# Kernel optimization log

Measured on AMD Instinct MI355X. Metric: run time of the kernel, lower is better.

Reference implementation:

```python
import jax, jax.numpy as jnp
import numpy as np

N_E = 1024
E_DIM = 256
N_TOK = 262144


def setup_inputs() -> dict:
    key = jax.random.key(0)
    kx, kw = jax.random.split(key)
    x = jax.random.normal(kx, (N_TOK, E_DIM), dtype=jnp.float32)
    # nn.Embedding weight init: uniform(-1/n_e, 1/n_e)
    emb = jax.random.uniform(kw, (N_E, E_DIM), dtype=jnp.float32,
                             minval=-1.0 / N_E, maxval=1.0 / N_E)
    return {"x": x, "emb": emb}


def reference(x, emb):
    # d[n, k] = ||x_n||^2 + ||e_k||^2 - 2 <x_n, e_k>   -> [N, n_e]
    d = (jnp.sum(x * x, axis=1, keepdims=True)
         + jnp.sum(emb * emb, axis=1)
         - 2.0 * jnp.matmul(x, emb.T))
    min_indices = jnp.argmin(d, axis=1)          # [N] int
    z_q = jnp.take(emb, min_indices, axis=0)     # [N, e_dim]
    return z_q, min_indices
```

## Files before the change

### kernel.cpp

```cpp
#include <hip/hip_runtime.h>


constexpr int N_E   = 1024;
constexpr int E_DIM = 256;
constexpr int N_TOK = 262144;
constexpr float THR = 3e-4f;
constexpr int RGRID  = 1024;
constexpr int RRANGE = N_TOK / RGRID;

typedef __attribute__((ext_vector_type(8))) short short8;
typedef __attribute__((ext_vector_type(4))) float f32x4;

__device__ __forceinline__ float sqf(float v) {
    float p = v * v;
    asm volatile("" : "+v"(p));
    return p;
}
__device__ __forceinline__ float pwb(const float* b, int n) {
    float U[8];
#pragma unroll
    for (int L = 0; L < 8; ++L) {
        float TL  = (sqf(b[L])     + sqf(b[16 + L])) + (sqf(b[32 + L]) + sqf(b[48 + L]));
        float TL8 = (sqf(b[8 + L]) + sqf(b[24 + L])) + (sqf(b[40 + L]) + sqf(b[56 + L]));
        U[L] = TL + TL8;
    }
    float V0 = U[0] + U[4], V1 = U[1] + U[5], V2 = U[2] + U[6], V3 = U[3] + U[7];
    float res = (V0 + V2) + (V1 + V3);
    for (int i = 64; i < n; ++i) res += sqf(b[i]);
    return res;
}
__device__ __forceinline__ float rowsq_exact(const float* r) {
    return sqf(r[0]) + (pwb(r + 1, 120) + (pwb(r + 121, 64) + pwb(r + 185, 71)));
}
__device__ __forceinline__ unsigned short f2bf(float f) {
    union { float f; unsigned u; } v; v.f = f;
    unsigned r = (v.u + 0x7FFF + ((v.u >> 16) & 1)) >> 16;
    return (unsigned short)r;
}

__global__ __launch_bounds__(64) void rowsq_kernel(const float* __restrict__ src,
                                                   float* __restrict__ dst) {
    __shared__ float rs[32][257];
    const int rowBase = blockIdx.x * 32;
    const int tid = threadIdx.x;
    const float4* s4 = reinterpret_cast<const float4*>(src);
    for (int i = tid; i < 32 * 64; i += 64) {
        int rr = i >> 6, c4 = i & 63;
        float4 v = s4[(size_t)(rowBase + rr) * 64 + c4];
        rs[rr][c4 * 4 + 0] = v.x;
        rs[rr][c4 * 4 + 1] = v.y;
        rs[rr][c4 * 4 + 2] = v.z;
        rs[rr][c4 * 4 + 3] = v.w;
    }
    __syncthreads();
    if (tid < 32) dst[rowBase + tid] = rowsq_exact(rs[tid]);
}

__global__ __launch_bounds__(256) void eprep_kernel(const float* __restrict__ emb,
                                                    short8* __restrict__ eb,
                                                    int* __restrict__ cnt) {
    int gid = blockIdx.x * 256 + threadIdx.x;
    if (gid == 0) *cnt = 0;
    int lane = gid & 63;
    int kc   = (gid >> 6) & 7;
    int nt   = gid >> 9;
    int cand = nt * 16 + (lane & 15);
    int k0   = kc * 32 + (lane >> 4) * 8;
    const float4* e4 = reinterpret_cast<const float4*>(emb);
    float4 a = e4[(size_t)cand * 64 + k0 / 4];
    float4 b = e4[(size_t)cand * 64 + k0 / 4 + 1];
    short8 o;
    o[0] = (short)f2bf(a.x); o[1] = (short)f2bf(a.y);
    o[2] = (short)f2bf(a.z); o[3] = (short)f2bf(a.w);
    o[4] = (short)f2bf(b.x); o[5] = (short)f2bf(b.y);
    o[6] = (short)f2bf(b.z); o[7] = (short)f2bf(b.w);
    eb[gid] = o;
}

__device__ __forceinline__ void top2_update(const f32x4& acc0, const f32x4& acc1,
                                            float Bv, int idx,
                                            float* m1, float* m2, int* i1) {
#pragma unroll
    for (int mt = 0; mt < 2; ++mt) {
        const f32x4& acc = mt ? acc1 : acc0;
#pragma unroll
        for (int r = 0; r < 4; ++r) {
            int t = mt * 4 + r;
            float s = Bv - 2.0f * acc[r];
            bool lt = s < m1[t];
            m2[t] = lt ? m1[t] : fminf(m2[t], s);
            m1[t] = lt ? s : m1[t];
            i1[t] = lt ? idx : i1[t];
        }
    }
}

__global__ __launch_bounds__(256, 4) void score_kernel(const float* __restrict__ x,
                                                       const float* __restrict__ emb,
                                                       const short8* __restrict__ eb,
                                                       const float* __restrict__ B,
                                                       float* __restrict__ zq,
                                                       float* __restrict__ outIdx,
                                                       int* __restrict__ cnt,
                                                       int* __restrict__ list,
                                                       int listCap) {
    __shared__ short8 esm[2][512];
    __shared__ int fidx[128];
    const int tid = threadIdx.x;
    const int wv  = tid >> 6;
    const int l   = tid & 63;
    const int col = l & 15;
    const int tokW = blockIdx.x * 128 + wv * 32;
    const float4* x4 = reinterpret_cast<const float4*>(x);

    short8 xf[2][8];
#pragma unroll
    for (int mt = 0; mt < 2; ++mt) {
        int row = tokW + mt * 16 + col;
#pragma unroll
        for (int kc = 0; kc < 8; ++kc) {
            const float4* p = x4 + (size_t)row * 64 + kc * 8 + (l >> 4) * 2;
            float4 a = p[0], b = p[1];
            short8 f;
            f[0] = (short)f2bf(a.x); f[1] = (short)f2bf(a.y);
            f[2] = (short)f2bf(a.z); f[3] = (short)f2bf(a.w);
            f[4] = (short)f2bf(b.x); f[5] = (short)f2bf(b.y);
            f[6] = (short)f2bf(b.z); f[7] = (short)f2bf(b.w);
            xf[mt][kc] = f;
        }
    }

    float m1[8], m2[8];
    int   i1[8];
#pragma unroll
    for (int t = 0; t < 8; ++t) { m1[t] = 3.4e38f; m2[t] = 3.4e38f; i1[t] = 0; }

    {
        short8 r0 = eb[tid];
        short8 r1 = eb[256 + tid];
        esm[0][tid]       = r0;
        esm[0][256 + tid] = r1;
    }
    __syncthreads();

    int cur = 0;
    for (int nt = 0; nt < 64; ++nt) {
        short8 p0, p1;
        if (nt < 63) {
            p0 = eb[(nt + 1) * 512 + tid];
            p1 = eb[(nt + 1) * 512 + 256 + tid];
        }
        float Bv = B[nt * 16 + col];
        f32x4 acc0 = {0.f, 0.f, 0.f, 0.f}, acc1 = acc0;
#pragma unroll
        for (int kc = 0; kc < 8; ++kc) {
            short8 ef = esm[cur][kc * 64 + l];
            acc0 = __builtin_amdgcn_mfma_f32_16x16x32_bf16(xf[0][kc], ef, acc0, 0, 0, 0);
            acc1 = __builtin_amdgcn_mfma_f32_16x16x32_bf16(xf[1][kc], ef, acc1, 0, 0, 0);
        }
        top2_update(acc0, acc1, Bv, nt * 16 + col, m1, m2, i1);
        if (nt < 63) {
            esm[cur ^ 1][tid]       = p0;
            esm[cur ^ 1][256 + tid] = p1;
            __syncthreads();
            cur ^= 1;
        }
    }

#pragma unroll
    for (int off = 1; off <= 8; off <<= 1) {
#pragma unroll
        for (int t = 0; t < 8; ++t) {
            float om1 = __shfl_xor(m1[t], off, 64);
            int   oi  = __shfl_xor(i1[t], off, 64);
            float om2 = __shfl_xor(m2[t], off, 64);
            float nm2 = fminf(fmaxf(m1[t], om1), fminf(m2[t], om2));
            if (om1 < m1[t] || (om1 == m1[t] && oi < i1[t])) { m1[t] = om1; i1[t] = oi; }
            m2[t] = nm2;
        }
    }

    if (col == 0) {
        int g = l >> 4;
#pragma unroll
        for (int mt = 0; mt < 2; ++mt)
#pragma unroll
            for (int r = 0; r < 4; ++r) {
                int t = mt * 4 + r;
                int token = tokW + mt * 16 + g * 4 + r;
                int fl = (m2[t] - m1[t] <= THR) ? 1 : 0;
                outIdx[token] = (float)(i1[t] + (fl ? N_E : 0));
                fidx[wv * 32 + mt * 16 + g * 4 + r] = i1[t];
                if (fl) {
                    int p = atomicAdd(cnt, 1);
                    if (p < listCap) list[p] = token;
                }
            }
    }
    __syncthreads();

    const float4* e4 = reinterpret_cast<const float4*>(emb);
    float4* zq4 = reinterpret_cast<float4*>(zq);
#pragma unroll
    for (int it = 0; it < 32; ++it) {
        int flat = it * 256 + tid;
        int t = flat >> 6, c = flat & 63;
        zq4[((size_t)blockIdx.x * 128 + t) * 64 + c] = e4[(size_t)fidx[t] * 64 + c];
    }
}

__device__ __forceinline__ void process_batch(const float4* x4, const float4* e4,
                                              const float* B, float4* zq4,
                                              float* outIdx,
                                              const int* toks, int m,
                                              float (*xs)[260], float* As,
                                              float (*wmin)[16], int (*widx)[16],
                                              int* bidx, int tid, int wv, int l) {
    for (int i = tid; i < 16 * 64; i += 256) {
        int t = i >> 6, c4 = i & 63;
        float4 v = {0.f, 0.f, 0.f, 0.f};
        if (t < m) v = x4[(size_t)toks[t] * 64 + c4];
        *reinterpret_cast<float4*>(&xs[t][c4 * 4]) = v;
    }
    __syncthreads();
    if (tid < 16) As[tid] = rowsq_exact(xs[tid]);
    __syncthreads();

    const float4* er[4];
#pragma unroll
    for (int j = 0; j < 4; ++j) er[j] = e4 + (size_t)(j * 256 + tid) * 64;

    float acc[16][4];
#pragma unroll
    for (int t = 0; t < 16; ++t)
#pragma unroll
        for (int j = 0; j < 4; ++j) acc[t][j] = 0.f;

    for (int ch = 0; ch < 32; ++ch) {
        float ee[4][8];
#pragma unroll
        for (int j = 0; j < 4; ++j) {
            float4 a = er[j][ch * 2 + 0];
            float4 b = er[j][ch * 2 + 1];
            ee[j][0] = a.x; ee[j][1] = a.y; ee[j][2] = a.z; ee[j][3] = a.w;
            ee[j][4] = b.x; ee[j][5] = b.y; ee[j][6] = b.z; ee[j][7] = b.w;
        }
#pragma unroll
        for (int t = 0; t < 16; ++t) {
            float4 xa = *reinterpret_cast<const float4*>(&xs[t][ch * 8 + 0]);
            float4 xb = *reinterpret_cast<const float4*>(&xs[t][ch * 8 + 4]);
            float xv[8] = {xa.x, xa.y, xa.z, xa.w, xb.x, xb.y, xb.z, xb.w};
#pragma unroll
            for (int j = 0; j < 4; ++j) {
                acc[t][j] += xv[0] * ee[j][0];
                acc[t][j] += xv[1] * ee[j][1];
                acc[t][j] += xv[2] * ee[j][2];
                acc[t][j] += xv[3] * ee[j][3];
                acc[t][j] += xv[4] * ee[j][4];
                acc[t][j] += xv[5] * ee[j][5];
                acc[t][j] += xv[6] * ee[j][6];
                acc[t][j] += xv[7] * ee[j][7];
            }
        }
    }

    float m1[16];
    int   i1[16];
#pragma unroll
    for (int t = 0; t < 16; ++t) { m1[t] = 3.4e38f; i1[t] = 0; }
#pragma unroll
    for (int j = 0; j < 4; ++j) {
        int c = j * 256 + tid;
        float Bc = B[c];
#pragma unroll
        for (int t = 0; t < 16; ++t) {
            float tt = As[t] + Bc;
            float s  = tt - 2.0f * acc[t][j];
            if (s < m1[t]) { m1[t] = s; i1[t] = c; }
        }
    }
#pragma unroll
    for (int off = 1; off <= 32; off <<= 1) {
#pragma unroll
        for (int t = 0; t < 16; ++t) {
            float om = __shfl_xor(m1[t], off, 64);
            int   oi = __shfl_xor(i1[t], off, 64);
            if (om < m1[t] || (om == m1[t] && oi < i1[t])) { m1[t] = om; i1[t] = oi; }
        }
    }
    if (l == 0) {
#pragma unroll
        for (int t = 0; t < 16; ++t) { wmin[wv][t] = m1[t]; widx[wv][t] = i1[t]; }
    }
    __syncthreads();
    if (tid < 16) {
        float bm = wmin[0][tid];
        int   bi = widx[0][tid];
#pragma unroll
        for (int w = 1; w < 4; ++w) {
            float om = wmin[w][tid];
            int   oi = widx[w][tid];
            if (om < bm || (om == bm && oi < bi)) { bm = om; bi = oi; }
        }
        bidx[tid] = bi;
        if (tid < m) outIdx[toks[tid]] = (float)bi;
    }
    __syncthreads();
    for (int i = tid; i < m * 64; i += 256) {
        int t = i >> 6, c4 = i & 63;
        zq4[(size_t)toks[t] * 64 + c4] = e4[(size_t)bidx[t] * 64 + c4];
    }
    __syncthreads();
}

__global__ __launch_bounds__(256) void recheck_kernel(const float* __restrict__ x,
                                                      const float* __restrict__ emb,
                                                      const float* __restrict__ B,
                                                      float* __restrict__ zq,
                                                      float* __restrict__ outIdx,
                                                      const int* __restrict__ cnt,
                                                      const int* __restrict__ list,
                                                      int listCap) {
    __shared__ float xs[16][260];
    __shared__ float As[16];
    __shared__ float wmin[4][16];
    __shared__ int   widx[4][16];
    __shared__ int   bidx[16];
    __shared__ int   lt[RRANGE];
    __shared__ int   kcount;

    const int tid = threadIdx.x;
    const int wv  = tid >> 6;
    const int l   = tid & 63;
    const float4* x4 = reinterpret_cast<const float4*>(x);
    const float4* e4 = reinterpret_cast<const float4*>(emb);
    float4* zq4 = reinterpret_cast<float4*>(zq);

    const int n = *cnt;
    if (n == 0) return;

    if (n <= listCap) {
        const int nsb = (n + 15) >> 4;
        for (int sb = blockIdx.x; sb < nsb; sb += gridDim.x) {
            const int m = (n - sb * 16 < 16) ? (n - sb * 16) : 16;
            if (tid < m) lt[tid] = list[sb * 16 + tid];
            __syncthreads();
            process_batch(x4, e4, B, zq4, outIdx, lt, m,
                          xs, As, wmin, widx, bidx, tid, wv, l);
        }
    } else {
        const int base = blockIdx.x * RRANGE;
        if (tid == 0) kcount = 0;
        __syncthreads();
        for (int i = tid; i < RRANGE; i += 256) {
            float v = outIdx[base + i];
            if (v >= (float)N_E) {
                int p = atomicAdd(&kcount, 1);
                lt[p] = base + i;
            }
        }
        __syncthreads();
        const int k = kcount;
        for (int sb = 0; sb < k; sb += 16) {
            const int m = (k - sb < 16) ? (k - sb) : 16;
            process_batch(x4, e4, B, zq4, outIdx, lt + sb, m,
                          xs, As, wmin, widx, bidx, tid, wv, l);
        }
    }
}

extern "C" void kernel_launch(void* const* d_in, const int* in_sizes, int n_in,
                              void* d_out, int out_size, void* d_ws, size_t ws_size,
                              hipStream_t stream) {
    const float* x   = (const float*)d_in[0];
    const float* emb = (const float*)d_in[1];
    float* out    = (float*)d_out;
    float* zq     = out;
    float* outIdx = out + (size_t)N_TOK * E_DIM;

    char* ws = (char*)d_ws;
    int*    cnt  = (int*)ws;
    float*  B    = (float*)(ws + 4096);
    short8* eb   = (short8*)(ws + 8192);
    int*    list = (int*)(ws + 8192 + 524288);
    long avail = (long)ws_size - (8192 + 524288);
    int listCap = avail > 0 ? (int)(avail / 4) : 0;
    if (listCap > N_TOK) listCap = N_TOK;

    eprep_kernel<<<128, 256, 0, stream>>>(emb, eb, cnt);
    rowsq_kernel<<<N_E / 32, 64, 0, stream>>>(emb, B);
    score_kernel<<<N_TOK / 128, 256, 0, stream>>>(x, emb, eb, B, zq, outIdx, cnt, list, listCap);
    recheck_kernel<<<RGRID, 256, 0, stream>>>(x, emb, B, zq, outIdx, cnt, list, listCap);
}
```

Measured before the change: 476.8 us.

## Cull recheck candidates with bf16 MFMA prefilter before exact fp32 rescoring

In the recheck pass, ambiguous tokens are first scored against all codes with bf16 MFMA. Only codes within a margin of the approximate minimum are kept as candidates, and those few are rescored exactly in fp32. This replaces a full fp32 distance computation over all 1024 codes for each flagged token. If any token has more than 64 candidates, the batch falls back to the full path, and the margin has to cover bf16 error for the result to stay exact.

```diff
diff --git a/kernel.cpp b/kernel.cpp
--- a/kernel.cpp
+++ b/kernel.cpp
@@ -4,9 +4,11 @@
 constexpr int N_E   = 1024;
 constexpr int E_DIM = 256;
 constexpr int N_TOK = 262144;
-constexpr float THR = 3e-4f;
+constexpr float THR  = 3e-4f;
+constexpr float CULL = 6e-4f;
 constexpr int RGRID  = 1024;
 constexpr int RRANGE = N_TOK / RGRID;
+constexpr int CMAX   = 64;
 
 typedef __attribute__((ext_vector_type(8))) short short8;
 typedef __attribute__((ext_vector_type(4))) float f32x4;
@@ -209,13 +211,13 @@
     }
 }
 
-__device__ __forceinline__ void process_batch(const float4* x4, const float4* e4,
-                                              const float* B, float4* zq4,
-                                              float* outIdx,
-                                              const int* toks, int m,
-                                              float (*xs)[260], float* As,
-                                              float (*wmin)[16], int (*widx)[16],
-                                              int* bidx, int tid, int wv, int l) {
+__device__ __forceinline__ void process_batch_full(const float4* x4, const float4* e4,
+                                                   const float* B, float4* zq4,
+                                                   float* outIdx,
+                                                   const int* toks, int m,
+                                                   float (*xs)[260], float* As,
+                                                   float (*wmin)[16], int (*widx)[16],
+                                                   int* bidx, int tid, int wv, int l) {
     for (int i = tid; i < 16 * 64; i += 256) {
         int t = i >> 6, c4 = i & 63;
         float4 v = {0.f, 0.f, 0.f, 0.f};
@@ -315,6 +317,7 @@
 
 __global__ __launch_bounds__(256) void recheck_kernel(const float* __restrict__ x,
                                                       const float* __restrict__ emb,
+                                                      const short8* __restrict__ eb,
                                                       const float* __restrict__ B,
                                                       float* __restrict__ zq,
                                                       float* __restrict__ outIdx,
@@ -328,10 +331,16 @@
     __shared__ int   bidx[16];
     __shared__ int   lt[RRANGE];
     __shared__ int   kcount;
+    __shared__ int   ccnt[16];
+    __shared__ int   clist[16][CMAX];
+    __shared__ float esc[16][CMAX];
+    __shared__ float bth[16];
+    __shared__ int   ovf;
 
     const int tid = threadIdx.x;
     const int wv  = tid >> 6;
     const int l   = tid & 63;
+    const int col = l & 15;
     const float4* x4 = reinterpret_cast<const float4*>(x);
     const float4* e4 = reinterpret_cast<const float4*>(emb);
     float4* zq4 = reinterpret_cast<float4*>(zq);
@@ -339,16 +348,7 @@
     const int n = *cnt;
     if (n == 0) return;
 
-    if (n <= listCap) {
-        const int nsb = (n + 15) >> 4;
-        for (int sb = blockIdx.x; sb < nsb; sb += gridDim.x) {
-            const int m = (n - sb * 16 < 16) ? (n - sb * 16) : 16;
-            if (tid < m) lt[tid] = list[sb * 16 + tid];
-            __syncthreads();
-            process_batch(x4, e4, B, zq4, outIdx, lt, m,
-                          xs, As, wmin, widx, bidx, tid, wv, l);
-        }
-    } else {
+    if (n > listCap) {
         const int base = blockIdx.x * RRANGE;
         if (tid == 0) kcount = 0;
         __syncthreads();
@@ -363,9 +363,136 @@
         const int k = kcount;
         for (int sb = 0; sb < k; sb += 16) {
             const int m = (k - sb < 16) ? (k - sb) : 16;
-            process_batch(x4, e4, B, zq4, outIdx, lt + sb, m,
-                          xs, As, wmin, widx, bidx, tid, wv, l);
-        }
+            process_batch_full(x4, e4, B, zq4, outIdx, lt + sb, m,
+                               xs, As, wmin, widx, bidx, tid, wv, l);
+        }
+        return;
+    }
+
+    const int nsb = (n + 15) >> 4;
+    for (int sb = blockIdx.x; sb < nsb; sb += gridDim.x) {
+        const int m = (n - sb * 16 < 16) ? (n - sb * 16) : 16;
+        if (tid < 16) {
+            lt[tid]   = (tid < m) ? list[sb * 16 + tid] : list[sb * 16];
+            ccnt[tid] = 0;
+        }
+        if (tid == 0) ovf = 0;
+        __syncthreads();
+
+        for (int i = tid; i < 16 * 64; i += 256) {
+            int t = i >> 6, c4 = i & 63;
+            float4 v = x4[(size_t)lt[t] * 64 + c4];
+            *reinterpret_cast<float4*>(&xs[t][c4 * 4]) = v;
+        }
+        __syncthreads();
+
+        short8 xf[8];
+#pragma unroll
+        for (int kc = 0; kc < 8; ++kc) {
+            const float4* p = x4 + (size_t)lt[col] * 64 + kc * 8 + (l >> 4) * 2;
+            float4 a = p[0], b = p[1];
+            short8 f;
+            f[0] = (short)f2bf(a.x); f[1] = (short)f2bf(a.y);
+            f[2] = (short)f2bf(a.z); f[3] = (short)f2bf(a.w);
+            f[4] = (short)f2bf(b.x); f[5] = (short)f2bf(b.y);
+            f[6] = (short)f2bf(b.z); f[7] = (short)f2bf(b.w);
+            xf[kc] = f;
+        }
+        f32x4 sc[16];
+#pragma unroll
+        for (int nt = 0; nt < 16; ++nt) {
+            const short8* ep = eb + (size_t)(wv * 16 + nt) * 512 + l;
+            f32x4 acc = {0.f, 0.f, 0.f, 0.f};
+#pragma unroll
+            for (int kc = 0; kc < 8; ++kc)
+                acc = __builtin_amdgcn_mfma_f32_16x16x32_bf16(xf[kc], ep[kc * 64], acc, 0, 0, 0);
+            sc[nt] = acc;
+        }
+        float m1loc[4] = {3.4e38f, 3.4e38f, 3.4e38f, 3.4e38f};
+#pragma unroll
+        for (int nt = 0; nt < 16; ++nt) {
+            float Bv = B[(wv * 16 + nt) * 16 + col];
+#pragma unroll
+            for (int r = 0; r < 4; ++r)
+                m1loc[r] = fminf(m1loc[r], Bv - 2.0f * sc[nt][r]);
+        }
+#pragma unroll
+        for (int off = 1; off <= 8; off <<= 1)
+#pragma unroll
+            for (int r = 0; r < 4; ++r)
+                m1loc[r] = fminf(m1loc[r], __shfl_xor(m1loc[r], off, 64));
+        if (col == 0) {
+#pragma unroll
+            for (int r = 0; r < 4; ++r) wmin[wv][(l >> 4) * 4 + r] = m1loc[r];
+        }
+        __syncthreads();
+        if (tid < 16) {
+            float bm = fminf(fminf(wmin[0][tid], wmin[1][tid]),
+                             fminf(wmin[2][tid], wmin[3][tid]));
+            bth[tid] = bm + CULL;
+            As[tid]  = rowsq_exact(xs[tid]);
+        }
+        __syncthreads();
+
+#pragma unroll
+        for (int nt = 0; nt < 16; ++nt) {
+            float Bv = B[(wv * 16 + nt) * 16 + col];
+#pragma unroll
+            for (int r = 0; r < 4; ++r) {
+                int t = (l >> 4) * 4 + r;
+                float s = Bv - 2.0f * sc[nt][r];
+                if (s <= bth[t]) {
+                    int p = atomicAdd(&ccnt[t], 1);
+                    if (p < CMAX) clist[t][p] = (wv * 16 + nt) * 16 + col;
+                    else atomicOr(&ovf, 1);
+                }
+            }
+        }
+        __syncthreads();
+
+        if (ovf) {
+            process_batch_full(x4, e4, B, zq4, outIdx, lt, m,
+                               xs, As, wmin, widx, bidx, tid, wv, l);
+            continue;
+        }
+
+        for (int i = tid; i < 16 * CMAX; i += 256) {
+            int t = i & 15, slot = i >> 4;
+            int kt = ccnt[t] < CMAX ? ccnt[t] : CMAX;
+            if (slot < kt) {
+                int c = clist[t][slot];
+                float acc = 0.f;
+                for (int d4 = 0; d4 < 64; ++d4) {
+                    float4 e = e4[(size_t)c * 64 + d4];
+                    acc += xs[t][d4 * 4 + 0] * e.x;
+                    acc += xs[t][d4 * 4 + 1] * e.y;
+                    acc += xs[t][d4 * 4 + 2] * e.z;
+                    acc += xs[t][d4 * 4 + 3] * e.w;
+                }
+                float tt = As[t] + B[c];
+                esc[t][slot] = tt - 2.0f * acc;
+            }
+        }
+        __syncthreads();
+
+        if (tid < 16) {
+            int kt = ccnt[tid] < CMAX ? ccnt[tid] : CMAX;
+            float best = 3.4e38f;
+            int   bi   = 0x7fffffff;
+            for (int slot = 0; slot < kt; ++slot) {
+                float s = esc[tid][slot];
+                int   c = clist[tid][slot];
+                if (s < best || (s == best && c < bi)) { best = s; bi = c; }
+            }
+            bidx[tid] = bi;
+            if (tid < m) outIdx[lt[tid]] = (float)bi;
+        }
+        __syncthreads();
+        for (int i = tid; i < m * 64; i += 256) {
+            int t = i >> 6, c4 = i & 63;
+            zq4[(size_t)lt[t] * 64 + c4] = e4[(size_t)bidx[t] * 64 + c4];
+        }
+        __syncthreads();
     }
 }
 
@@ -390,5 +517,5 @@
     eprep_kernel<<<128, 256, 0, stream>>>(emb, eb, cnt);
     rowsq_kernel<<<N_E / 32, 64, 0, stream>>>(emb, B);
     score_kernel<<<N_TOK / 128, 256, 0, stream>>>(x, emb, eb, B, zq, outIdx, cnt, list, listCap);
-    recheck_kernel<<<RGRID, 256, 0, stream>>>(x, emb, B, zq, outIdx, cnt, list, listCap);
-}
+    recheck_kernel<<<RGRID, 256, 0, stream>>>(x, emb, eb, B, zq, outIdx, cnt, list, listCap);
+}
```

Measured after the change: 599.4 us. +25.7%, slower.
